# Kernel optimization log

Measured on AMD Instinct MI355X. Metric: run time of the kernel, lower is better.

## Reference

```python
import jax, jax.numpy as jnp
import numpy as np

NUM_HEAD = 16

def setup_inputs() -> dict:
    rk = jax.random.key(0)
    k1, k2, k3, k4, k5 = jax.random.split(rk, 5)
    B, Sq, Skv, D = 4, 2048, 2048, 1024
    return {
        "query": jax.random.normal(k1, (B, Sq, D), dtype=jnp.float32),
        "key":   jax.random.normal(k2, (B, Skv, D), dtype=jnp.float32),
        "value": jax.random.normal(k3, (B, Skv, D), dtype=jnp.float32),
        "W": jax.random.normal(k4, (D, D), dtype=jnp.float32) * (D ** -0.5),
        "b": jax.random.normal(k5, (D,), dtype=jnp.float32) * 0.01,
    }

def reference(query, key, value, W, b):
    B, Sq, D = query.shape
    H = NUM_HEAD
    hd = D // H
    # chunk(num_head, -1) == split last dim into H contiguous heads
    q = query.reshape(B, Sq, H, hd)
    k = key.reshape(B, -1, H, hd)
    v = value.reshape(B, -1, H, hd)
    # scores[b,h,q,k] = (Q_h K_h^T) / sqrt(embedding_dim)  (full dim, per source)
    scores = jnp.einsum('bqhd,bkhd->bhqk', q, k) / jnp.sqrt(jnp.float32(D))
    # nn.Softmax(dim=1) on a [B, q, kv] matrix -> softmax over the QUERY axis
    attn = jax.nn.softmax(scores, axis=2)
    out = jnp.einsum('bhqk,bkhd->bqhd', attn, v).reshape(B, Sq, D)
    # final linear: x @ W^T + b
    return out @ W.T + b
```

## Files before the change

### kernel.cpp

```cpp
#include <hip/hip_runtime.h>

#define NH    16
#define HD    64
#define SQ    2048
#define SKV   2048
#define DM    1024

typedef __attribute__((ext_vector_type(8))) __bf16 bf16x8;
typedef __attribute__((ext_vector_type(4))) __bf16 bf16x4;
typedef __attribute__((ext_vector_type(4))) float  f32x4;

static __device__ __forceinline__ bf16x4 cvt4(float4 v) {
    bf16x4 r;
    r[0] = (__bf16)v.x; r[1] = (__bf16)v.y; r[2] = (__bf16)v.z; r[3] = (__bf16)v.w;
    return r;
}

__global__ void kprep(const float* __restrict__ src, __bf16* __restrict__ dst) {
    size_t g = (size_t)blockIdx.x * 256 + threadIdx.x;
    size_t o = g * 8;
    int c  = (int)(o & 63);
    int s  = (int)((o >> 6) & 2047);
    int bh = (int)(o >> 17);
    int b = bh >> 4, h = bh & 15;
    const float* p = src + ((size_t)(b * SQ + s)) * DM + h * HD + c;
    float4 v0 = *(const float4*)p;
    float4 v1 = *(const float4*)(p + 4);
    bf16x8 r;
    r[0] = (__bf16)v0.x; r[1] = (__bf16)v0.y; r[2] = (__bf16)v0.z; r[3] = (__bf16)v0.w;
    r[4] = (__bf16)v1.x; r[5] = (__bf16)v1.y; r[6] = (__bf16)v1.z; r[7] = (__bf16)v1.w;
    *(bf16x8*)(dst + o) = r;
}

__global__ void kconv_w(const float* __restrict__ W, __bf16* __restrict__ Wb) {
    int i = blockIdx.x * 256 + threadIdx.x;
    float4 v = *(const float4*)(W + (size_t)i * 4);
    *(bf16x4*)(Wb + (size_t)i * 4) = cvt4(v);
}

__global__ __launch_bounds__(256, 3) void kz(const __bf16* __restrict__ Qh,
                                             const __bf16* __restrict__ Kh,
                                             const float* __restrict__ v,
                                             __bf16* __restrict__ Vt) {
    const int kb = blockIdx.x;
    const int bh = blockIdx.y;
    const int b = bh >> 4, h = bh & 15;
    const int t = threadIdx.x;
    const int w = t >> 6, lane = t & 63;
    const int lo16 = lane & 15, quad = lane >> 4;

    __shared__ __bf16 Ks[256 * 72];
    __shared__ __bf16 Qs[64 * 72];
    __shared__ float  Zs[256];

    const __bf16* kbase = Kh + ((size_t)bh * SKV + kb * 256) * HD;
    const __bf16* qbase = Qh + (size_t)bh * SQ * HD;

#pragma unroll
    for (int i = 0; i < 8; ++i) {
        int idx = t + i * 256;
        int row = idx >> 3, ch = idx & 7;
        *(bf16x8*)(&Ks[row * 72 + ch * 8]) = *(const bf16x8*)(kbase + (size_t)idx * 8);
    }
    __syncthreads();

    bf16x8 bk[4][2];
#pragma unroll
    for (int nt = 0; nt < 4; ++nt)
#pragma unroll
        for (int dh = 0; dh < 2; ++dh)
            bk[nt][dh] = *(const bf16x8*)(&Ks[(w * 64 + nt * 16 + lo16) * 72 + dh * 32 + quad * 8]);

    float zacc[4] = {0.f, 0.f, 0.f, 0.f};

    for (int qt = 0; qt < 32; ++qt) {
        __syncthreads();
#pragma unroll
        for (int i = 0; i < 2; ++i) {
            int idx = t + i * 256;
            int row = idx >> 3, ch = idx & 7;
            *(bf16x8*)(&Qs[row * 72 + ch * 8]) =
                *(const bf16x8*)(qbase + (size_t)qt * 64 * HD + idx * 8);
        }
        __syncthreads();

#pragma unroll
        for (int mt = 0; mt < 4; ++mt) {
            bf16x8 aq0 = *(const bf16x8*)(&Qs[(mt * 16 + lo16) * 72 + quad * 8]);
            bf16x8 aq1 = *(const bf16x8*)(&Qs[(mt * 16 + lo16) * 72 + 32 + quad * 8]);
#pragma unroll
            for (int nt = 0; nt < 4; ++nt) {
                f32x4 acc = {0.f, 0.f, 0.f, 0.f};
                acc = __builtin_amdgcn_mfma_f32_16x16x32_bf16(aq0, bk[nt][0], acc, 0, 0, 0);
                acc = __builtin_amdgcn_mfma_f32_16x16x32_bf16(aq1, bk[nt][1], acc, 0, 0, 0);
                zacc[nt] += __expf(acc[0] * 0.03125f) + __expf(acc[1] * 0.03125f)
                          + __expf(acc[2] * 0.03125f) + __expf(acc[3] * 0.03125f);
            }
        }
    }

#pragma unroll
    for (int nt = 0; nt < 4; ++nt) {
        float s = zacc[nt];
        s += __shfl_xor(s, 16, 64);
        s += __shfl_xor(s, 32, 64);
        if (lane < 16) Zs[w * 64 + nt * 16 + lane] = s;
    }
    __syncthreads();

    {
        float rz = 1.0f / Zs[t];
        const float* vrow = v + ((size_t)(b * SKV) + kb * 256 + t) * DM + h * HD;
        size_t vtb = (size_t)bh * HD * SKV + kb * 256 + t;
#pragma unroll
        for (int dc = 0; dc < 4; ++dc) {
            float4 a0 = *(const float4*)(vrow + dc * 16 + 0);
            float4 a1 = *(const float4*)(vrow + dc * 16 + 4);
            float4 a2 = *(const float4*)(vrow + dc * 16 + 8);
            float4 a3 = *(const float4*)(vrow + dc * 16 + 12);
            float tmp[16] = {a0.x, a0.y, a0.z, a0.w, a1.x, a1.y, a1.z, a1.w,
                             a2.x, a2.y, a2.z, a2.w, a3.x, a3.y, a3.z, a3.w};
#pragma unroll
            for (int j = 0; j < 16; ++j)
                Vt[vtb + (size_t)(dc * 16 + j) * SKV] = (__bf16)(tmp[j] * rz);
        }
    }
}

__global__ __launch_bounds__(256, 2) void kattn(const __bf16* __restrict__ Qh,
                                                const __bf16* __restrict__ Kh,
                                                const __bf16* __restrict__ Vt,
                                                __bf16* __restrict__ O) {
    const int qb = blockIdx.x;
    const int bh = blockIdx.y;
    const int b = bh >> 4, h = bh & 15;
    const int t = threadIdx.x;
    const int w = t >> 6, lane = t & 63;
    const int lo16 = lane & 15, quad = lane >> 4;

    __shared__ __bf16 Ks[64 * 72];
    __shared__ __bf16 Vts[64 * 72];
    __shared__ __bf16 QE[256 * 72];

    const __bf16* qgbase = Qh + ((size_t)bh * SQ + qb * 256) * HD;
#pragma unroll
    for (int i = 0; i < 8; ++i) {
        int idx = t + i * 256;
        int row = idx >> 3, ch = idx & 7;
        *(bf16x8*)(&QE[row * 72 + ch * 8]) = *(const bf16x8*)(qgbase + (size_t)idx * 8);
    }
    __syncthreads();

    bf16x8 qf[4][2];
#pragma unroll
    for (int qt = 0; qt < 4; ++qt)
#pragma unroll
        for (int dh = 0; dh < 2; ++dh)
            qf[qt][dh] = *(const bf16x8*)(&QE[(w * 64 + qt * 16 + lo16) * 72 + dh * 32 + quad * 8]);

    f32x4 oacc[4][4];
    f32x4 zero = {0.f, 0.f, 0.f, 0.f};
#pragma unroll
    for (int qt = 0; qt < 4; ++qt)
#pragma unroll
        for (int nt = 0; nt < 4; ++nt)
            oacc[qt][nt] = zero;

    __bf16* Ew = &QE[w * 64 * 72];
    const __bf16* kgbase = Kh + (size_t)bh * SKV * HD;
    const __bf16* vtgbase = Vt + (size_t)bh * HD * SKV;

    for (int kt = 0; kt < 32; ++kt) {
        __syncthreads();
#pragma unroll
        for (int i = 0; i < 2; ++i) {
            int idx = t + i * 256;
            int row = idx >> 3, ch = idx & 7;
            *(bf16x8*)(&Ks[row * 72 + ch * 8]) =
                *(const bf16x8*)(kgbase + (size_t)kt * 64 * HD + idx * 8);
            *(bf16x8*)(&Vts[row * 72 + ch * 8]) =
                *(const bf16x8*)(vtgbase + (size_t)row * SKV + kt * 64 + ch * 8);
        }
        __syncthreads();

#pragma unroll
        for (int ktile = 0; ktile < 4; ++ktile) {
            bf16x8 ak0 = *(const bf16x8*)(&Ks[(ktile * 16 + lo16) * 72 + quad * 8]);
            bf16x8 ak1 = *(const bf16x8*)(&Ks[(ktile * 16 + lo16) * 72 + 32 + quad * 8]);
#pragma unroll
            for (int qt = 0; qt < 4; ++qt) {
                f32x4 s = zero;
                s = __builtin_amdgcn_mfma_f32_16x16x32_bf16(ak0, qf[qt][0], s, 0, 0, 0);
                s = __builtin_amdgcn_mfma_f32_16x16x32_bf16(ak1, qf[qt][1], s, 0, 0, 0);
                bf16x4 e;
                e[0] = (__bf16)__expf(s[0] * 0.03125f);
                e[1] = (__bf16)__expf(s[1] * 0.03125f);
                e[2] = (__bf16)__expf(s[2] * 0.03125f);
                e[3] = (__bf16)__expf(s[3] * 0.03125f);
                *(bf16x4*)(&Ew[(qt * 16 + lo16) * 72 + ktile * 16 + quad * 4]) = e;
            }
        }

#pragma unroll
        for (int kk2 = 0; kk2 < 2; ++kk2) {
            bf16x8 ae[4];
#pragma unroll
            for (int qt = 0; qt < 4; ++qt)
                ae[qt] = *(const bf16x8*)(&Ew[(qt * 16 + lo16) * 72 + kk2 * 32 + quad * 8]);
#pragma unroll
            for (int nt = 0; nt < 4; ++nt) {
                bf16x8 bv = *(const bf16x8*)(&Vts[(nt * 16 + lo16) * 72 + kk2 * 32 + quad * 8]);
#pragma unroll
                for (int qt = 0; qt < 4; ++qt)
                    oacc[qt][nt] = __builtin_amdgcn_mfma_f32_16x16x32_bf16(ae[qt], bv, oacc[qt][nt], 0, 0, 0);
            }
        }
    }

    size_t obase = ((size_t)(b * SQ) + qb * 256 + w * 64) * DM + h * HD;
#pragma unroll
    for (int qt = 0; qt < 4; ++qt)
#pragma unroll
        for (int nt = 0; nt < 4; ++nt)
#pragma unroll
            for (int r = 0; r < 4; ++r)
                O[obase + (size_t)(qt * 16 + quad * 4 + r) * DM + nt * 16 + lo16] =
                    (__bf16)oacc[qt][nt][r];
}

__global__ __launch_bounds__(256, 2) void kproj(const __bf16* __restrict__ A,
                                                const __bf16* __restrict__ Wb,
                                                const float* __restrict__ bias,
                                                float* __restrict__ out) {
    const int nb = blockIdx.x;
    const int mb = blockIdx.y;
    const int t = threadIdx.x;
    const int w = t >> 6, lane = t & 63;
    const int lo16 = lane & 15, quad = lane >> 4;
    const int wm = w & 1, wn = w >> 1;

    __shared__ __bf16 As[128 * 72];
    __shared__ __bf16 Bs[128 * 72];

    f32x4 acc[4][4];
    f32x4 zero = {0.f, 0.f, 0.f, 0.f};
#pragma unroll
    for (int mt = 0; mt < 4; ++mt)
#pragma unroll
        for (int nt = 0; nt < 4; ++nt)
            acc[mt][nt] = zero;

    const __bf16* abase = A + (size_t)(mb * 128) * DM;
    const __bf16* wbase = Wb + (size_t)(nb * 128) * DM;

    for (int kt = 0; kt < 16; ++kt) {
        __syncthreads();
#pragma unroll
        for (int i = 0; i < 4; ++i) {
            int idx = t + i * 256;
            int row = idx >> 3, ch = idx & 7;
            *(bf16x8*)(&As[row * 72 + ch * 8]) =
                *(const bf16x8*)(abase + (size_t)row * DM + kt * 64 + ch * 8);
            *(bf16x8*)(&Bs[row * 72 + ch * 8]) =
                *(const bf16x8*)(wbase + (size_t)row * DM + kt * 64 + ch * 8);
        }
        __syncthreads();

#pragma unroll
        for (int ks = 0; ks < 2; ++ks) {
            bf16x8 av[4], bv[4];
#pragma unroll
            for (int mt = 0; mt < 4; ++mt)
                av[mt] = *(const bf16x8*)(&As[(wm * 64 + mt * 16 + lo16) * 72 + ks * 32 + quad * 8]);
#pragma unroll
            for (int nt = 0; nt < 4; ++nt)
                bv[nt] = *(const bf16x8*)(&Bs[(wn * 64 + nt * 16 + lo16) * 72 + ks * 32 + quad * 8]);
#pragma unroll
            for (int mt = 0; mt < 4; ++mt)
#pragma unroll
                for (int nt = 0; nt < 4; ++nt)
                    acc[mt][nt] = __builtin_amdgcn_mfma_f32_16x16x32_bf16(av[mt], bv[nt], acc[mt][nt], 0, 0, 0);
        }
    }

    const int col0 = nb * 128 + wn * 64;
    const int row0 = mb * 128 + wm * 64;
#pragma unroll
    for (int nt = 0; nt < 4; ++nt) {
        float bb = bias[col0 + nt * 16 + lo16];
#pragma unroll
        for (int mt = 0; mt < 4; ++mt)
#pragma unroll
            for (int r = 0; r < 4; ++r)
                out[(size_t)(row0 + mt * 16 + quad * 4 + r) * DM + col0 + nt * 16 + lo16] =
                    acc[mt][nt][r] + bb;
    }
}

extern "C" void kernel_launch(void* const* d_in, const int* in_sizes, int n_in,
                              void* d_out, int out_size, void* d_ws, size_t ws_size,
                              hipStream_t stream) {
    const float* q    = (const float*)d_in[0];
    const float* k    = (const float*)d_in[1];
    const float* v    = (const float*)d_in[2];
    const float* W    = (const float*)d_in[3];
    const float* bias = (const float*)d_in[4];
    float* out = (float*)d_out;

    char* ws = (char*)d_ws;
    __bf16* Qh = (__bf16*)ws;
    __bf16* Kh = (__bf16*)(ws + (16u << 20));
    __bf16* Vt = (__bf16*)(ws + (32u << 20));
    __bf16* Wb = (__bf16*)(ws + (48u << 20));
    __bf16* O  = (__bf16*)(ws + (50u << 20));

    kprep  <<<dim3(4096), 256, 0, stream>>>(q, Qh);
    kprep  <<<dim3(4096), 256, 0, stream>>>(k, Kh);
    kconv_w<<<dim3(1024), 256, 0, stream>>>(W, Wb);
    kz     <<<dim3(8, 64), 256, 0, stream>>>(Qh, Kh, v, Vt);
    kattn  <<<dim3(8, 64), 256, 0, stream>>>(Qh, Kh, Vt, O);
    kproj  <<<dim3(8, 64), 256, 0, stream>>>(O, Wb, bias, out);
}
```

Measured before the change: 330.3 us.

## Use direct global-to-LDS async loads with XOR-swizzled unpadded shared tiles

```diff
diff --git a/kernel.cpp b/kernel.cpp
--- a/kernel.cpp
+++ b/kernel.cpp
@@ -9,6 +9,21 @@
 typedef __attribute__((ext_vector_type(8))) __bf16 bf16x8;
 typedef __attribute__((ext_vector_type(4))) __bf16 bf16x4;
 typedef __attribute__((ext_vector_type(4))) float  f32x4;
+
+#define ASYNC16(gp, lp)                                                        \
+    __builtin_amdgcn_global_load_lds(                                          \
+        (const __attribute__((address_space(1))) void*)(gp),                   \
+        (__attribute__((address_space(3))) void*)(lp), 16, 0, 0)
+
+#if __has_builtin(__builtin_amdgcn_exp2f)
+#define EXPS(x) __builtin_amdgcn_exp2f((x) * 0.04508422f)
+#else
+#define EXPS(x) __expf((x) * 0.03125f)
+#endif
+
+static __device__ __forceinline__ int swz(int row, int chunk) {
+    return (row << 6) + (((chunk) ^ (row & 7)) << 3);
+}
 
 static __device__ __forceinline__ bf16x4 cvt4(float4 v) {
     bf16x4 r;
@@ -42,15 +57,16 @@
                                              const __bf16* __restrict__ Kh,
                                              const float* __restrict__ v,
                                              __bf16* __restrict__ Vt) {
-    const int kb = blockIdx.x;
-    const int bh = blockIdx.y;
+    const int bh = blockIdx.x;
+    const int kb = blockIdx.y;
     const int b = bh >> 4, h = bh & 15;
     const int t = threadIdx.x;
     const int w = t >> 6, lane = t & 63;
     const int lo16 = lane & 15, quad = lane >> 4;
-
-    __shared__ __bf16 Ks[256 * 72];
-    __shared__ __bf16 Qs[64 * 72];
+    const int wub = (t & 192) << 3;
+
+    __shared__ __bf16 Ks[256 * 64];
+    __shared__ __bf16 Qs[64 * 64];
     __shared__ float  Zs[256];
 
     const __bf16* kbase = Kh + ((size_t)bh * SKV + kb * 256) * HD;
@@ -58,9 +74,10 @@
 
 #pragma unroll
     for (int i = 0; i < 8; ++i) {
-        int idx = t + i * 256;
-        int row = idx >> 3, ch = idx & 7;
-        *(bf16x8*)(&Ks[row * 72 + ch * 8]) = *(const bf16x8*)(kbase + (size_t)idx * 8);
+        int ci = i * 256 + t;
+        int row = ci >> 3;
+        int c = (ci & 7) ^ (row & 7);
+        ASYNC16(kbase + row * 64 + c * 8, &Ks[i * 2048 + wub]);
     }
     __syncthreads();
 
@@ -69,7 +86,7 @@
     for (int nt = 0; nt < 4; ++nt)
 #pragma unroll
         for (int dh = 0; dh < 2; ++dh)
-            bk[nt][dh] = *(const bf16x8*)(&Ks[(w * 64 + nt * 16 + lo16) * 72 + dh * 32 + quad * 8]);
+            bk[nt][dh] = *(const bf16x8*)(&Ks[swz(w * 64 + nt * 16 + lo16, dh * 4 + quad)]);
 
     float zacc[4] = {0.f, 0.f, 0.f, 0.f};
 
@@ -77,24 +94,23 @@
         __syncthreads();
 #pragma unroll
         for (int i = 0; i < 2; ++i) {
-            int idx = t + i * 256;
-            int row = idx >> 3, ch = idx & 7;
-            *(bf16x8*)(&Qs[row * 72 + ch * 8]) =
-                *(const bf16x8*)(qbase + (size_t)qt * 64 * HD + idx * 8);
+            int ci = i * 256 + t;
+            int row = ci >> 3;
+            int c = (ci & 7) ^ (row & 7);
+            ASYNC16(qbase + (size_t)qt * 64 * HD + row * 64 + c * 8, &Qs[i * 2048 + wub]);
         }
         __syncthreads();
 
 #pragma unroll
         for (int mt = 0; mt < 4; ++mt) {
-            bf16x8 aq0 = *(const bf16x8*)(&Qs[(mt * 16 + lo16) * 72 + quad * 8]);
-            bf16x8 aq1 = *(const bf16x8*)(&Qs[(mt * 16 + lo16) * 72 + 32 + quad * 8]);
+            bf16x8 aq0 = *(const bf16x8*)(&Qs[swz(mt * 16 + lo16, quad)]);
+            bf16x8 aq1 = *(const bf16x8*)(&Qs[swz(mt * 16 + lo16, 4 + quad)]);
 #pragma unroll
             for (int nt = 0; nt < 4; ++nt) {
                 f32x4 acc = {0.f, 0.f, 0.f, 0.f};
                 acc = __builtin_amdgcn_mfma_f32_16x16x32_bf16(aq0, bk[nt][0], acc, 0, 0, 0);
                 acc = __builtin_amdgcn_mfma_f32_16x16x32_bf16(aq1, bk[nt][1], acc, 0, 0, 0);
-                zacc[nt] += __expf(acc[0] * 0.03125f) + __expf(acc[1] * 0.03125f)
-                          + __expf(acc[2] * 0.03125f) + __expf(acc[3] * 0.03125f);
+                zacc[nt] += EXPS(acc[0]) + EXPS(acc[1]) + EXPS(acc[2]) + EXPS(acc[3]);
             }
         }
     }
@@ -127,27 +143,29 @@
     }
 }
 
-__global__ __launch_bounds__(256, 2) void kattn(const __bf16* __restrict__ Qh,
+__global__ __launch_bounds__(256, 3) void kattn(const __bf16* __restrict__ Qh,
                                                 const __bf16* __restrict__ Kh,
                                                 const __bf16* __restrict__ Vt,
                                                 __bf16* __restrict__ O) {
-    const int qb = blockIdx.x;
-    const int bh = blockIdx.y;
+    const int bh = blockIdx.x;
+    const int qb = blockIdx.y;
     const int b = bh >> 4, h = bh & 15;
     const int t = threadIdx.x;
     const int w = t >> 6, lane = t & 63;
     const int lo16 = lane & 15, quad = lane >> 4;
-
-    __shared__ __bf16 Ks[64 * 72];
-    __shared__ __bf16 Vts[64 * 72];
-    __shared__ __bf16 QE[256 * 72];
+    const int wub = (t & 192) << 3;
+
+    __shared__ __bf16 Ks[64 * 64];
+    __shared__ __bf16 Vts[64 * 64];
+    __shared__ __bf16 QE[256 * 64];
 
     const __bf16* qgbase = Qh + ((size_t)bh * SQ + qb * 256) * HD;
 #pragma unroll
     for (int i = 0; i < 8; ++i) {
-        int idx = t + i * 256;
-        int row = idx >> 3, ch = idx & 7;
-        *(bf16x8*)(&QE[row * 72 + ch * 8]) = *(const bf16x8*)(qgbase + (size_t)idx * 8);
+        int ci = i * 256 + t;
+        int row = ci >> 3;
+        int c = (ci & 7) ^ (row & 7);
+        ASYNC16(qgbase + row * 64 + c * 8, &QE[i * 2048 + wub]);
     }
     __syncthreads();
 
@@ -156,7 +174,7 @@
     for (int qt = 0; qt < 4; ++qt)
 #pragma unroll
         for (int dh = 0; dh < 2; ++dh)
-            qf[qt][dh] = *(const bf16x8*)(&QE[(w * 64 + qt * 16 + lo16) * 72 + dh * 32 + quad * 8]);
+            qf[qt][dh] = *(const bf16x8*)(&QE[swz(w * 64 + qt * 16 + lo16, dh * 4 + quad)]);
 
     f32x4 oacc[4][4];
     f32x4 zero = {0.f, 0.f, 0.f, 0.f};
@@ -166,7 +184,7 @@
         for (int nt = 0; nt < 4; ++nt)
             oacc[qt][nt] = zero;
 
-    __bf16* Ew = &QE[w * 64 * 72];
+    __bf16* Ew = &QE[w * 64 * 64];
     const __bf16* kgbase = Kh + (size_t)bh * SKV * HD;
     const __bf16* vtgbase = Vt + (size_t)bh * HD * SKV;
 
@@ -174,30 +192,31 @@
         __syncthreads();
 #pragma unroll
         for (int i = 0; i < 2; ++i) {
-            int idx = t + i * 256;
-            int row = idx >> 3, ch = idx & 7;
-            *(bf16x8*)(&Ks[row * 72 + ch * 8]) =
-                *(const bf16x8*)(kgbase + (size_t)kt * 64 * HD + idx * 8);
-            *(bf16x8*)(&Vts[row * 72 + ch * 8]) =
-                *(const bf16x8*)(vtgbase + (size_t)row * SKV + kt * 64 + ch * 8);
+            int ci = i * 256 + t;
+            int row = ci >> 3;
+            int c = (ci & 7) ^ (row & 7);
+            ASYNC16(kgbase + (size_t)kt * 64 * HD + row * 64 + c * 8, &Ks[i * 2048 + wub]);
+            ASYNC16(vtgbase + (size_t)row * SKV + kt * 64 + c * 8, &Vts[i * 2048 + wub]);
         }
         __syncthreads();
 
 #pragma unroll
         for (int ktile = 0; ktile < 4; ++ktile) {
-            bf16x8 ak0 = *(const bf16x8*)(&Ks[(ktile * 16 + lo16) * 72 + quad * 8]);
-            bf16x8 ak1 = *(const bf16x8*)(&Ks[(ktile * 16 + lo16) * 72 + 32 + quad * 8]);
+            bf16x8 ak0 = *(const bf16x8*)(&Ks[swz(ktile * 16 + lo16, quad)]);
+            bf16x8 ak1 = *(const bf16x8*)(&Ks[swz(ktile * 16 + lo16, 4 + quad)]);
 #pragma unroll
             for (int qt = 0; qt < 4; ++qt) {
                 f32x4 s = zero;
                 s = __builtin_amdgcn_mfma_f32_16x16x32_bf16(ak0, qf[qt][0], s, 0, 0, 0);
                 s = __builtin_amdgcn_mfma_f32_16x16x32_bf16(ak1, qf[qt][1], s, 0, 0, 0);
                 bf16x4 e;
-                e[0] = (__bf16)__expf(s[0] * 0.03125f);
-                e[1] = (__bf16)__expf(s[1] * 0.03125f);
-                e[2] = (__bf16)__expf(s[2] * 0.03125f);
-                e[3] = (__bf16)__expf(s[3] * 0.03125f);
-                *(bf16x4*)(&Ew[(qt * 16 + lo16) * 72 + ktile * 16 + quad * 4]) = e;
+                e[0] = (__bf16)EXPS(s[0]);
+                e[1] = (__bf16)EXPS(s[1]);
+                e[2] = (__bf16)EXPS(s[2]);
+                e[3] = (__bf16)EXPS(s[3]);
+                int er = qt * 16 + lo16;
+                *(bf16x4*)(&Ew[(er << 6) + ((((2 * ktile + (quad >> 1))) ^ (er & 7)) << 3)
+                               + (quad & 1) * 4]) = e;
             }
         }
 
@@ -206,10 +225,10 @@
             bf16x8 ae[4];
 #pragma unroll
             for (int qt = 0; qt < 4; ++qt)
-                ae[qt] = *(const bf16x8*)(&Ew[(qt * 16 + lo16) * 72 + kk2 * 32 + quad * 8]);
+                ae[qt] = *(const bf16x8*)(&Ew[swz(qt * 16 + lo16, kk2 * 4 + quad)]);
 #pragma unroll
             for (int nt = 0; nt < 4; ++nt) {
-                bf16x8 bv = *(const bf16x8*)(&Vts[(nt * 16 + lo16) * 72 + kk2 * 32 + quad * 8]);
+                bf16x8 bv = *(const bf16x8*)(&Vts[swz(nt * 16 + lo16, kk2 * 4 + quad)]);
 #pragma unroll
                 for (int qt = 0; qt < 4; ++qt)
                     oacc[qt][nt] = __builtin_amdgcn_mfma_f32_16x16x32_bf16(ae[qt], bv, oacc[qt][nt], 0, 0, 0);
@@ -228,7 +247,7 @@
                     (__bf16)oacc[qt][nt][r];
 }
 
-__global__ __launch_bounds__(256, 2) void kproj(const __bf16* __restrict__ A,
+__global__ __launch_bounds__(256, 3) void kproj(const __bf16* __restrict__ A,
                                                 const __bf16* __restrict__ Wb,
                                                 const float* __restrict__ bias,
                                                 float* __restrict__ out) {
@@ -238,9 +257,10 @@
     const int w = t >> 6, lane = t & 63;
     const int lo16 = lane & 15, quad = lane >> 4;
     const int wm = w & 1, wn = w >> 1;
-
-    __shared__ __bf16 As[128 * 72];
-    __shared__ __bf16 Bs[128 * 72];
+    const int wub = (t & 192) << 3;
+
+    __shared__ __bf16 As[128 * 64];
+    __shared__ __bf16 Bs[128 * 64];
 
     f32x4 acc[4][4];
     f32x4 zero = {0.f, 0.f, 0.f, 0.f};
@@ -257,12 +277,11 @@
         __syncthreads();
 #pragma unroll
         for (int i = 0; i < 4; ++i) {
-            int idx = t + i * 256;
-            int row = idx >> 3, ch = idx & 7;
-            *(bf16x8*)(&As[row * 72 + ch * 8]) =
-                *(const bf16x8*)(abase + (size_t)row * DM + kt * 64 + ch * 8);
-            *(bf16x8*)(&Bs[row * 72 + ch * 8]) =
-                *(const bf16x8*)(wbase + (size_t)row * DM + kt * 64 + ch * 8);
+            int ci = i * 256 + t;
+            int row = ci >> 3;
+            int c = (ci & 7) ^ (row & 7);
+            ASYNC16(abase + (size_t)row * DM + kt * 64 + c * 8, &As[i * 2048 + wub]);
+            ASYNC16(wbase + (size_t)row * DM + kt * 64 + c * 8, &Bs[i * 2048 + wub]);
         }
         __syncthreads();
 
@@ -271,10 +290,10 @@
             bf16x8 av[4], bv[4];
 #pragma unroll
             for (int mt = 0; mt < 4; ++mt)
-                av[mt] = *(const bf16x8*)(&As[(wm * 64 + mt * 16 + lo16) * 72 + ks * 32 + quad * 8]);
+                av[mt] = *(const bf16x8*)(&As[swz(wm * 64 + mt * 16 + lo16, ks * 4 + quad)]);
 #pragma unroll
             for (int nt = 0; nt < 4; ++nt)
-                bv[nt] = *(const bf16x8*)(&Bs[(wn * 64 + nt * 16 + lo16) * 72 + ks * 32 + quad * 8]);
+                bv[nt] = *(const bf16x8*)(&Bs[swz(wn * 64 + nt * 16 + lo16, ks * 4 + quad)]);
 #pragma unroll
             for (int mt = 0; mt < 4; ++mt)
 #pragma unroll
@@ -317,7 +336,7 @@
     kprep  <<<dim3(4096), 256, 0, stream>>>(q, Qh);
     kprep  <<<dim3(4096), 256, 0, stream>>>(k, Kh);
     kconv_w<<<dim3(1024), 256, 0, stream>>>(W, Wb);
-    kz     <<<dim3(8, 64), 256, 0, stream>>>(Qh, Kh, v, Vt);
-    kattn  <<<dim3(8, 64), 256, 0, stream>>>(Qh, Kh, Vt, O);
+    kz     <<<dim3(64, 8), 256, 0, stream>>>(Qh, Kh, v, Vt);
+    kattn  <<<dim3(64, 8), 256, 0, stream>>>(Qh, Kh, Vt, O);
     kproj  <<<dim3(8, 64), 256, 0, stream>>>(O, Wb, bias, out);
 }
```

Result: faster. 298.5 us (-9.6%).
